# Performance work log

Hardware: AMD Instinct MI355X
Metric: run time of the kernel (lower is better)

Reference implementation:

```python
import jax, jax.numpy as jnp
import numpy as np

B, T, D = 2, 2048, 1024
H = 16
DH = D // H            # 64, per-head dim
C = 128                # d_kv_compress
ROPE_BASE = 10000.0


def _rope_cos_sin(t_len, d_head, dtype):
    # freqs: (T, d_head/2); emb = cat(freqs, freqs) -> (T, d_head)
    inv_freq = 1.0 / (ROPE_BASE ** (jnp.arange(0, d_head, 2, dtype=jnp.float32) / d_head))
    freqs = jnp.arange(t_len, dtype=jnp.float32)[:, None] * inv_freq[None, :]
    emb = jnp.concatenate([freqs, freqs], axis=-1)
    return jnp.cos(emb).astype(dtype), jnp.sin(emb).astype(dtype)


def _rotate_half(x):
    x1, x2 = jnp.split(x, 2, axis=-1)
    return jnp.concatenate([-x2, x1], axis=-1)


def _apply_rope(x, cos, sin):
    # x: (B,H,T,DH); cos/sin: (T,DH)
    return x * cos[None, None] + _rotate_half(x) * sin[None, None]


def setup_inputs() -> dict:
    key = jax.random.key(0)
    ks = jax.random.split(key, 12)
    s = 0.02
    return {
        "x": jax.random.normal(ks[0], (B, T, D), dtype=jnp.float32),
        "w_dk": jax.random.normal(ks[1], (D, C), dtype=jnp.float32) * s,
        "b_dk": jnp.zeros((C,), dtype=jnp.float32),
        "w_dv": jax.random.normal(ks[2], (D, C), dtype=jnp.float32) * s,
        "b_dv": jnp.zeros((C,), dtype=jnp.float32),
        "w_uk": jax.random.normal(ks[3], (C, D), dtype=jnp.float32) * s,
        "b_uk": jnp.zeros((D,), dtype=jnp.float32),
        "w_uv": jax.random.normal(ks[4], (C, D), dtype=jnp.float32) * s,
        "b_uv": jnp.zeros((D,), dtype=jnp.float32),
        "w_o": jax.random.normal(ks[5], (D, D), dtype=jnp.float32) * s,
        "b_o": jnp.zeros((D,), dtype=jnp.float32),
    }


def reference(x, w_dk, b_dk, w_dv, b_dv, w_uk, b_uk, w_uv, b_uv, w_o, b_o):
    Bx, Tx, Dx = x.shape
    # low-rank KV compression then up-projection
    c_k = x @ w_dk + b_dk                      # (B,T,C)
    c_v = x @ w_dv + b_dv                      # (B,T,C)
    k = c_k @ w_uk + b_uk                      # (B,T,D)
    v = c_v @ w_uv + b_uv                      # (B,T,D)

    def split_heads(t):  # (B,T,D) -> (B,H,T,DH)
        return t.reshape(Bx, Tx, H, DH).transpose(0, 2, 1, 3)

    q = split_heads(x)
    k = split_heads(k)
    v = split_heads(v)

    cos, sin = _rope_cos_sin(Tx, DH, x.dtype)
    q = _apply_rope(q, cos, sin)
    k = _apply_rope(k, cos, sin)

    scale = 1.0 / np.sqrt(DH)
    attn = jnp.einsum('bhid,bhjd->bhij', q, k) * scale
    attn = jax.nn.softmax(attn, axis=-1)
    out = jnp.einsum('bhij,bhjd->bhid', attn, v)   # (B,H,T,DH)
    out = out.transpose(0, 2, 1, 3).reshape(Bx, Tx, Dx)
    return out @ w_o + b_o
```

## Files before the change

### kernel.cpp

```cpp
#include <hip/hip_runtime.h>
#include <math.h>

constexpr int kB  = 2;
constexpr int kT  = 2048;
constexpr int kD  = 1024;
constexpr int kH  = 16;
constexpr int kDH = 64;
constexpr int kC  = 128;
constexpr int kM  = kB * kT;
constexpr int kBH = kB * kH;

#define LOG10000_OVER_32 0.28782313662425575f

typedef unsigned short ushort_t;
using short8 = __attribute__((ext_vector_type(8))) short;
using f32x4  = __attribute__((ext_vector_type(4))) float;

__device__ inline ushort_t f2bf(float f) {
    unsigned int u = __float_as_uint(f);
    unsigned int r = (u + 0x7fffu + ((u >> 16) & 1u)) >> 16;
    return (ushort_t)r;
}

__device__ inline short8 cvt8(const float* p) {
    float4 f0 = *reinterpret_cast<const float4*>(p);
    float4 f1 = *reinterpret_cast<const float4*>(p + 4);
    short8 v;
    v[0] = (short)f2bf(f0.x); v[1] = (short)f2bf(f0.y);
    v[2] = (short)f2bf(f0.z); v[3] = (short)f2bf(f0.w);
    v[4] = (short)f2bf(f1.x); v[5] = (short)f2bf(f1.y);
    v[6] = (short)f2bf(f1.z); v[7] = (short)f2bf(f1.w);
    return v;
}

__global__ __launch_bounds__(256)
void wtrans(const float* __restrict__ w_dk, const float* __restrict__ w_dv,
            const float* __restrict__ w_uk, const float* __restrict__ w_uv,
            const float* __restrict__ w_o,
            ushort_t* __restrict__ dkT, ushort_t* __restrict__ dvT,
            ushort_t* __restrict__ ukT, ushort_t* __restrict__ uvT,
            ushort_t* __restrict__ oT) {
    const float* src; ushort_t* dst; int R, C;
    switch (blockIdx.z) {
        case 0: src = w_dk; dst = dkT; R = kD; C = kC; break;
        case 1: src = w_dv; dst = dvT; R = kD; C = kC; break;
        case 2: src = w_uk; dst = ukT; R = kC; C = kD; break;
        case 3: src = w_uv; dst = uvT; R = kC; C = kD; break;
        default: src = w_o; dst = oT;  R = kD; C = kD; break;
    }
    int c0 = blockIdx.x * 32, r0 = blockIdx.y * 32;
    if (c0 >= C || r0 >= R) return;

    __shared__ float Tl[32][33];
    int tx = threadIdx.x & 31, ty = threadIdx.x >> 5;
#pragma unroll
    for (int i = 0; i < 4; ++i)
        Tl[ty + 8 * i][tx] = src[(size_t)(r0 + ty + 8 * i) * C + c0 + tx];
    __syncthreads();
#pragma unroll
    for (int i = 0; i < 4; ++i)
        dst[(size_t)(c0 + ty + 8 * i) * R + r0 + tx] = f2bf(Tl[tx][ty + 8 * i]);
}

template<bool AF32, int MODE0, int MODE1>
__global__ __launch_bounds__(256)
void gemm_mfma(const void* __restrict__ A0_, const void* __restrict__ A1_,
               const ushort_t* __restrict__ Wt0, const float* __restrict__ bias0, void* __restrict__ C0,
               const ushort_t* __restrict__ Wt1, const float* __restrict__ bias1, void* __restrict__ C1,
               int M, int N, int K) {
    constexpr int LDT = 40;
    __shared__ __align__(16) ushort_t As[128 * LDT];
    __shared__ __align__(16) ushort_t Bs[128 * LDT];

    const void*     A    = blockIdx.z ? A1_ : A0_;
    const ushort_t* Wt   = blockIdx.z ? Wt1 : Wt0;
    const float*    bias = blockIdx.z ? bias1 : bias0;
    void*           Cc   = blockIdx.z ? C1 : C0;
    const int       mode = blockIdx.z ? MODE1 : MODE0;

    const int tid  = threadIdx.x;
    const int wave = tid >> 6, lane = tid & 63;
    const int g = lane >> 4, cl = lane & 15;
    const int m0 = blockIdx.y * 128, n0 = blockIdx.x * 128;
    const int wm = (wave >> 1) * 64, wn = (wave & 1) * 64;

    const int ar = tid >> 1;
    const int ac = (tid & 1) * 16;

    f32x4 acc[4][4] = {};

    for (int k0 = 0; k0 < K; k0 += 32) {
        if constexpr (AF32) {
            const float* Af = (const float*)A + (size_t)(m0 + ar) * K + k0 + ac;
            *reinterpret_cast<short8*>(&As[ar * LDT + ac])     = cvt8(Af);
            *reinterpret_cast<short8*>(&As[ar * LDT + ac + 8]) = cvt8(Af + 8);
        } else {
            const ushort_t* Ab = (const ushort_t*)A + (size_t)(m0 + ar) * K + k0 + ac;
            *reinterpret_cast<short8*>(&As[ar * LDT + ac])     = *reinterpret_cast<const short8*>(Ab);
            *reinterpret_cast<short8*>(&As[ar * LDT + ac + 8]) = *reinterpret_cast<const short8*>(Ab + 8);
        }
        {
            const ushort_t* Wb = Wt + (size_t)(n0 + ar) * K + k0 + ac;
            *reinterpret_cast<short8*>(&Bs[ar * LDT + ac])     = *reinterpret_cast<const short8*>(Wb);
            *reinterpret_cast<short8*>(&Bs[ar * LDT + ac + 8]) = *reinterpret_cast<const short8*>(Wb + 8);
        }
        __syncthreads();

        short8 a[4], b[4];
#pragma unroll
        for (int mi = 0; mi < 4; ++mi)
            a[mi] = *reinterpret_cast<const short8*>(&As[(wm + mi * 16 + cl) * LDT + g * 8]);
#pragma unroll
        for (int ni = 0; ni < 4; ++ni)
            b[ni] = *reinterpret_cast<const short8*>(&Bs[(wn + ni * 16 + cl) * LDT + g * 8]);
#pragma unroll
        for (int mi = 0; mi < 4; ++mi)
#pragma unroll
            for (int ni = 0; ni < 4; ++ni)
                acc[mi][ni] = __builtin_amdgcn_mfma_f32_16x16x32_bf16(a[mi], b[ni], acc[mi][ni], 0, 0, 0);
        __syncthreads();
    }

#pragma unroll
    for (int mi = 0; mi < 4; ++mi) {
#pragma unroll
        for (int ni = 0; ni < 4; ++ni) {
            const int mb = m0 + wm + mi * 16 + 4 * g;
            const int nn = n0 + wn + ni * 16 + cl;
            const float bv = bias[nn];
            if (mode == 0) {
#pragma unroll
                for (int r = 0; r < 4; ++r)
                    ((float*)Cc)[(size_t)(mb + r) * N + nn] = acc[mi][ni][r] + bv;
            } else if (mode == 3) {
#pragma unroll
                for (int r = 0; r < 4; ++r)
                    ((ushort_t*)Cc)[(size_t)(mb + r) * N + nn] = f2bf(acc[mi][ni][r] + bv);
            } else if (mode == 1) {
                const int h = nn >> 6, d = nn & (kDH - 1);
#pragma unroll
                for (int r = 0; r < 4; ++r) {
                    int m = mb + r;
                    int bb = m >> 11, t = m & (kT - 1);
                    ((float*)Cc)[(((size_t)bb * kH + h) * kT + t) * kDH + d] = acc[mi][ni][r] + bv;
                }
            } else {
                const int h = nn >> 6, d = nn & (kDH - 1);
                const int bb = mb >> 11, t0 = mb & (kT - 1);
                uint2 u;
                u.x = (unsigned int)f2bf(acc[mi][ni][0] + bv) | ((unsigned int)f2bf(acc[mi][ni][1] + bv) << 16);
                u.y = (unsigned int)f2bf(acc[mi][ni][2] + bv) | ((unsigned int)f2bf(acc[mi][ni][3] + bv) << 16);
                ushort_t* vt = (ushort_t*)Cc;
                *reinterpret_cast<uint2*>(&vt[(((size_t)bb * kH + h) * kDH + d) * kT + t0]) = u;
            }
        }
    }
}

__global__ __launch_bounds__(256)
void rope_split_q(const float* __restrict__ x, ushort_t* __restrict__ q_bf) {
    int idx = blockIdx.x * 256 + threadIdx.x;
    int i = idx & 31;
    int h = (idx >> 5) & (kH - 1);
    int t = (idx >> 9) & (kT - 1);
    int b = idx >> 20;

    const float* xp = x + ((size_t)(b * kT + t)) * kD + h * kDH;
    float x1 = xp[i];
    float x2 = xp[i + 32];

    float inv_freq = expf(-(float)i * LOG10000_OVER_32);
    float ang = (float)t * inv_freq;
    float s, c;
    sincosf(ang, &s, &c);

    ushort_t* qp = q_bf + (((size_t)(b * kH + h)) * kT + t) * kDH;
    qp[i]      = f2bf((x1 * c - x2 * s) * 0.125f);
    qp[i + 32] = f2bf((x2 * c + x1 * s) * 0.125f);
}

__global__ __launch_bounds__(256)
void rope_k_bf(const float* __restrict__ k_r, ushort_t* __restrict__ k_bf) {
    int idx = blockIdx.x * 256 + threadIdx.x;
    int i  = idx & 31;
    int t  = (idx >> 5) & (kT - 1);
    int bh = idx >> 16;

    const float* kp = k_r + ((size_t)bh * kT + t) * kDH;
    float k1 = kp[i];
    float k2 = kp[i + 32];

    float inv_freq = expf(-(float)i * LOG10000_OVER_32);
    float ang = (float)t * inv_freq;
    float s, c;
    sincosf(ang, &s, &c);

    ushort_t* op = k_bf + ((size_t)bh * kT + t) * kDH;
    op[i]      = f2bf(k1 * c - k2 * s);
    op[i + 32] = f2bf(k2 * c + k1 * s);
}

__global__ __launch_bounds__(256)
void attn_mfma(const ushort_t* __restrict__ q_bf, const ushort_t* __restrict__ k_bf,
               const ushort_t* __restrict__ vt_bf, ushort_t* __restrict__ att_bf) {
    constexpr int LDK = 72;
    constexpr int LDV = 40;
    const int blk  = blockIdx.x;
    const int bh   = (blk & 7) * 4 + ((blk >> 3) & 3);
    const int qt   = blk >> 5;
    const int tid  = threadIdx.x;
    const int wave = tid >> 6;
    const int lane = tid & 63;
    const int g = lane >> 4, c = lane & 15;
    const int qbase = qt * 64 + wave * 16;

    __shared__ __align__(16) ushort_t Ks[32 * LDK];
    __shared__ __align__(16) ushort_t Vs[64 * LDV];
    __shared__ __align__(16) ushort_t P_lds[4][16][32];
    ushort_t (*P)[32] = P_lds[wave];

    const ushort_t* qp = q_bf + ((size_t)bh * kT + qbase) * kDH;
    short8 qa0 = *reinterpret_cast<const short8*>(qp + (size_t)c * kDH + g * 8);
    short8 qa1 = *reinterpret_cast<const short8*>(qp + (size_t)c * kDH + g * 8 + 32);

    const ushort_t* kb = k_bf + (size_t)bh * kT * kDH;
    const ushort_t* vb = vt_bf + (size_t)bh * kDH * kT;

    const int kr_ = tid >> 3, kc_ = (tid & 7) * 8;
    const int vr_ = tid >> 2, vc_ = (tid & 3) * 8;

    f32x4 acc[4] = {};
    float lsum[4] = {0.f, 0.f, 0.f, 0.f};

    for (int kt = 0; kt < kT; kt += 32) {
        *reinterpret_cast<short8*>(&Ks[kr_ * LDK + kc_]) =
            *reinterpret_cast<const short8*>(&kb[(size_t)(kt + kr_) * kDH + kc_]);
        *reinterpret_cast<short8*>(&Vs[vr_ * LDV + vc_]) =
            *reinterpret_cast<const short8*>(&vb[(size_t)vr_ * kT + kt + vc_]);
        __syncthreads();

        short8 k00 = *reinterpret_cast<const short8*>(&Ks[c * LDK + g * 8]);
        short8 k01 = *reinterpret_cast<const short8*>(&Ks[c * LDK + 32 + g * 8]);
        short8 k10 = *reinterpret_cast<const short8*>(&Ks[(16 + c) * LDK + g * 8]);
        short8 k11 = *reinterpret_cast<const short8*>(&Ks[(16 + c) * LDK + 32 + g * 8]);

        f32x4 z = {0.f, 0.f, 0.f, 0.f};
        f32x4 s0 = __builtin_amdgcn_mfma_f32_16x16x32_bf16(qa0, k00, z, 0, 0, 0);
        s0 = __builtin_amdgcn_mfma_f32_16x16x32_bf16(qa1, k01, s0, 0, 0, 0);
        f32x4 s1 = __builtin_amdgcn_mfma_f32_16x16x32_bf16(qa0, k10, z, 0, 0, 0);
        s1 = __builtin_amdgcn_mfma_f32_16x16x32_bf16(qa1, k11, s1, 0, 0, 0);

        float p0[4], p1[4];
#pragma unroll
        for (int r = 0; r < 4; ++r) {
            p0[r] = __expf(s0[r]);
            p1[r] = __expf(s1[r]);
            lsum[r] += p0[r] + p1[r];
        }

#pragma unroll
        for (int r = 0; r < 4; ++r) {
            P[4 * g + r][c]      = f2bf(p0[r]);
            P[4 * g + r][16 + c] = f2bf(p1[r]);
        }
        short8 pa = *reinterpret_cast<const short8*>(&P[c][g * 8]);

#pragma unroll
        for (int n = 0; n < 4; ++n) {
            short8 vf = *reinterpret_cast<const short8*>(&Vs[(16 * n + c) * LDV + g * 8]);
            acc[n] = __builtin_amdgcn_mfma_f32_16x16x32_bf16(pa, vf, acc[n], 0, 0, 0);
        }
        __syncthreads();
    }

#pragma unroll
    for (int off = 1; off < 16; off <<= 1)
#pragma unroll
        for (int r = 0; r < 4; ++r) lsum[r] += __shfl_xor(lsum[r], off, 64);

    const int b = bh >> 4, h = bh & (kH - 1);
#pragma unroll
    for (int r = 0; r < 4; ++r) {
        float inv_l = 1.0f / lsum[r];
        size_t row = (size_t)(b * kT + qbase + 4 * g + r) * kD + h * kDH;
#pragma unroll
        for (int n = 0; n < 4; ++n)
            att_bf[row + 16 * n + c] = f2bf(acc[n][r] * inv_l);
    }
}

extern "C" void kernel_launch(void* const* d_in, const int* in_sizes, int n_in,
                              void* d_out, int out_size, void* d_ws, size_t ws_size,
                              hipStream_t stream) {
    const float* x    = (const float*)d_in[0];
    const float* w_dk = (const float*)d_in[1];
    const float* b_dk = (const float*)d_in[2];
    const float* w_dv = (const float*)d_in[3];
    const float* b_dv = (const float*)d_in[4];
    const float* w_uk = (const float*)d_in[5];
    const float* b_uk = (const float*)d_in[6];
    const float* w_uv = (const float*)d_in[7];
    const float* b_uv = (const float*)d_in[8];
    const float* w_o  = (const float*)d_in[9];
    const float* b_o  = (const float*)d_in[10];
    float* out = (float*)d_out;

    char* w = (char*)d_ws;
    float*    k_r    = (float*)w;     w += (size_t)kM * kD * 4;
    ushort_t* q_bf   = (ushort_t*)w;  w += (size_t)kM * kD * 2;
    ushort_t* k_bf   = (ushort_t*)w;  w += (size_t)kM * kD * 2;
    ushort_t* vt_bf  = (ushort_t*)w;  w += (size_t)kM * kD * 2;
    ushort_t* att_bf = (ushort_t*)w;  w += (size_t)kM * kD * 2;
    ushort_t* ckbf   = (ushort_t*)w;  w += (size_t)kM * kC * 2;
    ushort_t* cvbf   = (ushort_t*)w;  w += (size_t)kM * kC * 2;
    ushort_t* dkT    = (ushort_t*)w;  w += (size_t)kC * kD * 2;
    ushort_t* dvT    = (ushort_t*)w;  w += (size_t)kC * kD * 2;
    ushort_t* ukT    = (ushort_t*)w;  w += (size_t)kD * kC * 2;
    ushort_t* uvT    = (ushort_t*)w;  w += (size_t)kD * kC * 2;
    ushort_t* oT     = (ushort_t*)w;  w += (size_t)kD * kD * 2;

    dim3 blk(256);

    wtrans<<<dim3(32, 32, 5), blk, 0, stream>>>(w_dk, w_dv, w_uk, w_uv, w_o,
                                                dkT, dvT, ukT, uvT, oT);

    gemm_mfma<true, 3, 3><<<dim3(kC / 128, kM / 128, 2), blk, 0, stream>>>(
        x, x, dkT, b_dk, ckbf, dvT, b_dv, cvbf, kM, kC, kD);

    gemm_mfma<false, 1, 2><<<dim3(kD / 128, kM / 128, 2), blk, 0, stream>>>(
        ckbf, cvbf, ukT, b_uk, k_r, uvT, b_uv, vt_bf, kM, kD, kC);

    rope_split_q<<<(kB * kT * kH * 32) / 256, blk, 0, stream>>>(x, q_bf);
    rope_k_bf<<<(kB * kH * kT * 32) / 256, blk, 0, stream>>>(k_r, k_bf);

    attn_mfma<<<dim3(kT / 64 * kBH), blk, 0, stream>>>(q_bf, k_bf, vt_bf, att_bf);

    gemm_mfma<false, 0, 0><<<dim3(kD / 128, kM / 128, 1), blk, 0, stream>>>(
        att_bf, att_bf, oT, b_o, out, oT, b_o, out, kM, kD, kD);
}
```

Before: 255.0 us.

## Fuse K RoPE into up-projection epilogue, use sincos table, widen attention tiles

Precomputes a cos/sin table once in the weight-transpose kernel. The K up-projection GEMM now applies RoPE and writes bf16 directly, which removes the fp32 k_r buffer and the separate rope_k kernel. The q scale is folded with log2(e) so softmax can use exp2f. The attention kernel handles 32 query rows per wave (128 per block) so each K/V tile loaded into shared memory is reused twice, and the custom bf16 rounding is replaced by the library conversion. Softmax still skips max subtraction, so overflow risk remains, and the larger per-wave tile adds register pressure.

```diff
diff --git a/kernel.cpp b/kernel.cpp
--- a/kernel.cpp
+++ b/kernel.cpp
@@ -1,4 +1,5 @@
 #include <hip/hip_runtime.h>
+#include <hip/hip_bf16.h>
 #include <math.h>
 
 constexpr int kB  = 2;
@@ -11,15 +12,15 @@
 constexpr int kBH = kB * kH;
 
 #define LOG10000_OVER_32 0.28782313662425575f
+#define QSCALE 0.1803368801111773f
 
 typedef unsigned short ushort_t;
 using short8 = __attribute__((ext_vector_type(8))) short;
 using f32x4  = __attribute__((ext_vector_type(4))) float;
 
 __device__ inline ushort_t f2bf(float f) {
-    unsigned int u = __float_as_uint(f);
-    unsigned int r = (u + 0x7fffu + ((u >> 16) & 1u)) >> 16;
-    return (ushort_t)r;
+    __hip_bfloat16 h = __float2bfloat16(f);
+    return *reinterpret_cast<ushort_t*>(&h);
 }
 
 __device__ inline short8 cvt8(const float* p) {
@@ -39,7 +40,18 @@
             const float* __restrict__ w_o,
             ushort_t* __restrict__ dkT, ushort_t* __restrict__ dvT,
             ushort_t* __restrict__ ukT, ushort_t* __restrict__ uvT,
-            ushort_t* __restrict__ oT) {
+            ushort_t* __restrict__ oT, float2* __restrict__ tab) {
+    if (blockIdx.z == 5) {
+        int flat = blockIdx.y * 32 + blockIdx.x;
+        if (flat >= kT / 8) return;
+        int t = flat * 8 + (threadIdx.x >> 5);
+        int i = threadIdx.x & 31;
+        float inv_freq = expf(-(float)i * LOG10000_OVER_32);
+        float s, c;
+        sincosf((float)t * inv_freq, &s, &c);
+        tab[t * 32 + i] = make_float2(c, s);
+        return;
+    }
     const float* src; ushort_t* dst; int R, C;
     switch (blockIdx.z) {
         case 0: src = w_dk; dst = dkT; R = kD; C = kC; break;
@@ -67,7 +79,7 @@
 void gemm_mfma(const void* __restrict__ A0_, const void* __restrict__ A1_,
                const ushort_t* __restrict__ Wt0, const float* __restrict__ bias0, void* __restrict__ C0,
                const ushort_t* __restrict__ Wt1, const float* __restrict__ bias1, void* __restrict__ C1,
-               int M, int N, int K) {
+               const float2* __restrict__ tab, int M, int N, int K) {
     constexpr int LDT = 40;
     __shared__ __align__(16) ushort_t As[128 * LDT];
     __shared__ __align__(16) ushort_t Bs[128 * LDT];
@@ -123,6 +135,25 @@
 
 #pragma unroll
     for (int mi = 0; mi < 4; ++mi) {
+        if (mode == 4) {
+            const int h = (n0 + wn) >> 6;
+#pragma unroll
+            for (int r = 0; r < 4; ++r) {
+                const int m = m0 + wm + mi * 16 + 4 * g + r;
+                const int bb = m >> 11, t = m & (kT - 1);
+                ushort_t* kp = (ushort_t*)Cc + (((size_t)bb * kH + h) * kT + t) * kDH;
+#pragma unroll
+                for (int pr = 0; pr < 2; ++pr) {
+                    const int i = pr * 16 + cl;
+                    float2 cs = tab[t * 32 + i];
+                    float v1 = acc[mi][pr][r]     + bias[n0 + wn + pr * 16 + cl];
+                    float v2 = acc[mi][pr + 2][r] + bias[n0 + wn + (pr + 2) * 16 + cl];
+                    kp[i]      = f2bf(v1 * cs.x - v2 * cs.y);
+                    kp[i + 32] = f2bf(v2 * cs.x + v1 * cs.y);
+                }
+            }
+            continue;
+        }
 #pragma unroll
         for (int ni = 0; ni < 4; ++ni) {
             const int mb = m0 + wm + mi * 16 + 4 * g;
@@ -136,14 +167,6 @@
 #pragma unroll
                 for (int r = 0; r < 4; ++r)
                     ((ushort_t*)Cc)[(size_t)(mb + r) * N + nn] = f2bf(acc[mi][ni][r] + bv);
-            } else if (mode == 1) {
-                const int h = nn >> 6, d = nn & (kDH - 1);
-#pragma unroll
-                for (int r = 0; r < 4; ++r) {
-                    int m = mb + r;
-                    int bb = m >> 11, t = m & (kT - 1);
-                    ((float*)Cc)[(((size_t)bb * kH + h) * kT + t) * kDH + d] = acc[mi][ni][r] + bv;
-                }
             } else {
                 const int h = nn >> 6, d = nn & (kDH - 1);
                 const int bb = mb >> 11, t0 = mb & (kT - 1);
@@ -158,7 +181,8 @@
 }
 
 __global__ __launch_bounds__(256)
-void rope_split_q(const float* __restrict__ x, ushort_t* __restrict__ q_bf) {
+void rope_split_q(const float* __restrict__ x, const float2* __restrict__ tab,
+                  ushort_t* __restrict__ q_bf) {
     int idx = blockIdx.x * 256 + threadIdx.x;
     int i = idx & 31;
     int h = (idx >> 5) & (kH - 1);
@@ -168,36 +192,11 @@
     const float* xp = x + ((size_t)(b * kT + t)) * kD + h * kDH;
     float x1 = xp[i];
     float x2 = xp[i + 32];
-
-    float inv_freq = expf(-(float)i * LOG10000_OVER_32);
-    float ang = (float)t * inv_freq;
-    float s, c;
-    sincosf(ang, &s, &c);
+    float2 cs = tab[t * 32 + i];
 
     ushort_t* qp = q_bf + (((size_t)(b * kH + h)) * kT + t) * kDH;
-    qp[i]      = f2bf((x1 * c - x2 * s) * 0.125f);
-    qp[i + 32] = f2bf((x2 * c + x1 * s) * 0.125f);
-}
-
-__global__ __launch_bounds__(256)
-void rope_k_bf(const float* __restrict__ k_r, ushort_t* __restrict__ k_bf) {
-    int idx = blockIdx.x * 256 + threadIdx.x;
-    int i  = idx & 31;
-    int t  = (idx >> 5) & (kT - 1);
-    int bh = idx >> 16;
-
-    const float* kp = k_r + ((size_t)bh * kT + t) * kDH;
-    float k1 = kp[i];
-    float k2 = kp[i + 32];
-
-    float inv_freq = expf(-(float)i * LOG10000_OVER_32);
-    float ang = (float)t * inv_freq;
-    float s, c;
-    sincosf(ang, &s, &c);
-
-    ushort_t* op = k_bf + ((size_t)bh * kT + t) * kDH;
-    op[i]      = f2bf(k1 * c - k2 * s);
-    op[i + 32] = f2bf(k2 * c + k1 * s);
+    qp[i]      = f2bf((x1 * cs.x - x2 * cs.y) * QSCALE);
+    qp[i + 32] = f2bf((x2 * cs.x + x1 * cs.y) * QSCALE);
 }
 
 __global__ __launch_bounds__(256)
@@ -205,6 +204,7 @@
                const ushort_t* __restrict__ vt_bf, ushort_t* __restrict__ att_bf) {
     constexpr int LDK = 72;
     constexpr int LDV = 40;
+    constexpr int LDP = 36;
     const int blk  = blockIdx.x;
     const int bh   = (blk & 7) * 4 + ((blk >> 3) & 3);
     const int qt   = blk >> 5;
@@ -212,16 +212,20 @@
     const int wave = tid >> 6;
     const int lane = tid & 63;
     const int g = lane >> 4, c = lane & 15;
-    const int qbase = qt * 64 + wave * 16;
+    const int qbase = qt * 128 + wave * 32;
 
     __shared__ __align__(16) ushort_t Ks[32 * LDK];
     __shared__ __align__(16) ushort_t Vs[64 * LDV];
-    __shared__ __align__(16) ushort_t P_lds[4][16][32];
-    ushort_t (*P)[32] = P_lds[wave];
+    __shared__ __align__(16) ushort_t P_lds[4][32 * LDP];
+    ushort_t* P = P_lds[wave];
 
     const ushort_t* qp = q_bf + ((size_t)bh * kT + qbase) * kDH;
-    short8 qa0 = *reinterpret_cast<const short8*>(qp + (size_t)c * kDH + g * 8);
-    short8 qa1 = *reinterpret_cast<const short8*>(qp + (size_t)c * kDH + g * 8 + 32);
+    short8 qa[2][2];
+#pragma unroll
+    for (int qi = 0; qi < 2; ++qi)
+#pragma unroll
+        for (int f = 0; f < 2; ++f)
+            qa[qi][f] = *reinterpret_cast<const short8*>(qp + (size_t)(qi * 16 + c) * kDH + f * 32 + g * 8);
 
     const ushort_t* kb = k_bf + (size_t)bh * kT * kDH;
     const ushort_t* vb = vt_bf + (size_t)bh * kDH * kT;
@@ -229,8 +233,8 @@
     const int kr_ = tid >> 3, kc_ = (tid & 7) * 8;
     const int vr_ = tid >> 2, vc_ = (tid & 3) * 8;
 
-    f32x4 acc[4] = {};
-    float lsum[4] = {0.f, 0.f, 0.f, 0.f};
+    f32x4 acc[2][4] = {};
+    float lsum[2][4] = {};
 
     for (int kt = 0; kt < kT; kt += 32) {
         *reinterpret_cast<short8*>(&Ks[kr_ * LDK + kc_]) =
@@ -239,54 +243,70 @@
             *reinterpret_cast<const short8*>(&vb[(size_t)vr_ * kT + kt + vc_]);
         __syncthreads();
 
-        short8 k00 = *reinterpret_cast<const short8*>(&Ks[c * LDK + g * 8]);
-        short8 k01 = *reinterpret_cast<const short8*>(&Ks[c * LDK + 32 + g * 8]);
-        short8 k10 = *reinterpret_cast<const short8*>(&Ks[(16 + c) * LDK + g * 8]);
-        short8 k11 = *reinterpret_cast<const short8*>(&Ks[(16 + c) * LDK + 32 + g * 8]);
+        short8 kf[2][2];
+#pragma unroll
+        for (int kj = 0; kj < 2; ++kj)
+#pragma unroll
+            for (int f = 0; f < 2; ++f)
+                kf[kj][f] = *reinterpret_cast<const short8*>(&Ks[(kj * 16 + c) * LDK + f * 32 + g * 8]);
 
         f32x4 z = {0.f, 0.f, 0.f, 0.f};
-        f32x4 s0 = __builtin_amdgcn_mfma_f32_16x16x32_bf16(qa0, k00, z, 0, 0, 0);
-        s0 = __builtin_amdgcn_mfma_f32_16x16x32_bf16(qa1, k01, s0, 0, 0, 0);
-        f32x4 s1 = __builtin_amdgcn_mfma_f32_16x16x32_bf16(qa0, k10, z, 0, 0, 0);
-        s1 = __builtin_amdgcn_mfma_f32_16x16x32_bf16(qa1, k11, s1, 0, 0, 0);
-
-        float p0[4], p1[4];
+        f32x4 s[2][2];
+#pragma unroll
+        for (int qi = 0; qi < 2; ++qi)
+#pragma unroll
+            for (int kj = 0; kj < 2; ++kj) {
+                s[qi][kj] = __builtin_amdgcn_mfma_f32_16x16x32_bf16(qa[qi][0], kf[kj][0], z, 0, 0, 0);
+                s[qi][kj] = __builtin_amdgcn_mfma_f32_16x16x32_bf16(qa[qi][1], kf[kj][1], s[qi][kj], 0, 0, 0);
+            }
+
+#pragma unroll
+        for (int qi = 0; qi < 2; ++qi)
+#pragma unroll
+            for (int kj = 0; kj < 2; ++kj)
+#pragma unroll
+                for (int r = 0; r < 4; ++r) {
+                    float p = exp2f(s[qi][kj][r]);
+                    lsum[qi][r] += p;
+                    P[(qi * 16 + 4 * g + r) * LDP + kj * 16 + c] = f2bf(p);
+                }
+
+        short8 pa[2];
+#pragma unroll
+        for (int qi = 0; qi < 2; ++qi)
+            pa[qi] = *reinterpret_cast<const short8*>(&P[(qi * 16 + c) * LDP + g * 8]);
+
+        short8 vf[4];
+#pragma unroll
+        for (int n = 0; n < 4; ++n)
+            vf[n] = *reinterpret_cast<const short8*>(&Vs[(16 * n + c) * LDV + g * 8]);
+#pragma unroll
+        for (int qi = 0; qi < 2; ++qi)
+#pragma unroll
+            for (int n = 0; n < 4; ++n)
+                acc[qi][n] = __builtin_amdgcn_mfma_f32_16x16x32_bf16(pa[qi], vf[n], acc[qi][n], 0, 0, 0);
+        __syncthreads();
+    }
+
+#pragma unroll
+    for (int off = 1; off < 16; off <<= 1)
+#pragma unroll
+        for (int qi = 0; qi < 2; ++qi)
+#pragma unroll
+            for (int r = 0; r < 4; ++r)
+                lsum[qi][r] += __shfl_xor(lsum[qi][r], off, 64);
+
+    const int b = bh >> 4, h = bh & (kH - 1);
+#pragma unroll
+    for (int qi = 0; qi < 2; ++qi)
 #pragma unroll
         for (int r = 0; r < 4; ++r) {
-            p0[r] = __expf(s0[r]);
-            p1[r] = __expf(s1[r]);
-            lsum[r] += p0[r] + p1[r];
-        }
-
-#pragma unroll
-        for (int r = 0; r < 4; ++r) {
-            P[4 * g + r][c]      = f2bf(p0[r]);
-            P[4 * g + r][16 + c] = f2bf(p1[r]);
-        }
-        short8 pa = *reinterpret_cast<const short8*>(&P[c][g * 8]);
-
-#pragma unroll
-        for (int n = 0; n < 4; ++n) {
-            short8 vf = *reinterpret_cast<const short8*>(&Vs[(16 * n + c) * LDV + g * 8]);
-            acc[n] = __builtin_amdgcn_mfma_f32_16x16x32_bf16(pa, vf, acc[n], 0, 0, 0);
-        }
-        __syncthreads();
-    }
-
-#pragma unroll
-    for (int off = 1; off < 16; off <<= 1)
-#pragma unroll
-        for (int r = 0; r < 4; ++r) lsum[r] += __shfl_xor(lsum[r], off, 64);
-
-    const int b = bh >> 4, h = bh & (kH - 1);
-#pragma unroll
-    for (int r = 0; r < 4; ++r) {
-        float inv_l = 1.0f / lsum[r];
-        size_t row = (size_t)(b * kT + qbase + 4 * g + r) * kD + h * kDH;
-#pragma unroll
-        for (int n = 0; n < 4; ++n)
-            att_bf[row + 16 * n + c] = f2bf(acc[n][r] * inv_l);
-    }
+            float inv_l = 1.0f / lsum[qi][r];
+            size_t row = (size_t)(b * kT + qbase + qi * 16 + 4 * g + r) * kD + h * kDH;
+#pragma unroll
+            for (int n = 0; n < 4; ++n)
+                att_bf[row + 16 * n + c] = f2bf(acc[qi][n][r] * inv_l);
+        }
 }
 
 extern "C" void kernel_launch(void* const* d_in, const int* in_sizes, int n_in,
@@ -306,7 +326,6 @@
     float* out = (float*)d_out;
 
     char* w = (char*)d_ws;
-    float*    k_r    = (float*)w;     w += (size_t)kM * kD * 4;
     ushort_t* q_bf   = (ushort_t*)w;  w += (size_t)kM * kD * 2;
     ushort_t* k_bf   = (ushort_t*)w;  w += (size_t)kM * kD * 2;
     ushort_t* vt_bf  = (ushort_t*)w;  w += (size_t)kM * kD * 2;
@@ -318,23 +337,23 @@
     ushort_t* ukT    = (ushort_t*)w;  w += (size_t)kD * kC * 2;
     ushort_t* uvT    = (ushort_t*)w;  w += (size_t)kD * kC * 2;
     ushort_t* oT     = (ushort_t*)w;  w += (size_t)kD * kD * 2;
+    float2*   tab    = (float2*)w;    w += (size_t)kT * 32 * 8;
 
     dim3 blk(256);
 
-    wtrans<<<dim3(32, 32, 5), blk, 0, stream>>>(w_dk, w_dv, w_uk, w_uv, w_o,
-                                                dkT, dvT, ukT, uvT, oT);
+    wtrans<<<dim3(32, 32, 6), blk, 0, stream>>>(w_dk, w_dv, w_uk, w_uv, w_o,
+                                                dkT, dvT, ukT, uvT, oT, tab);
 
     gemm_mfma<true, 3, 3><<<dim3(kC / 128, kM / 128, 2), blk, 0, stream>>>(
-        x, x, dkT, b_dk, ckbf, dvT, b_dv, cvbf, kM, kC, kD);
-
-    gemm_mfma<false, 1, 2><<<dim3(kD / 128, kM / 128, 2), blk, 0, stream>>>(
-        ckbf, cvbf, ukT, b_uk, k_r, uvT, b_uv, vt_bf, kM, kD, kC);
-
-    rope_split_q<<<(kB * kT * kH * 32) / 256, blk, 0, stream>>>(x, q_bf);
-    rope_k_bf<<<(kB * kH * kT * 32) / 256, blk, 0, stream>>>(k_r, k_bf);
-
-    attn_mfma<<<dim3(kT / 64 * kBH), blk, 0, stream>>>(q_bf, k_bf, vt_bf, att_bf);
+        x, x, dkT, b_dk, ckbf, dvT, b_dv, cvbf, nullptr, kM, kC, kD);
+
+    gemm_mfma<false, 4, 2><<<dim3(kD / 128, kM / 128, 2), blk, 0, stream>>>(
+        ckbf, cvbf, ukT, b_uk, k_bf, uvT, b_uv, vt_bf, tab, kM, kD, kC);
+
+    rope_split_q<<<(kB * kT * kH * 32) / 256, blk, 0, stream>>>(x, tab, q_bf);
+
+    attn_mfma<<<dim3(kT / 128 * kBH), blk, 0, stream>>>(q_bf, k_bf, vt_bf, att_bf);
 
     gemm_mfma<false, 0, 0><<<dim3(kD / 128, kM / 128, 1), blk, 0, stream>>>(
-        att_bf, att_bf, oT, b_o, out, oT, b_o, out, kM, kD, kD);
-}
+        att_bf, att_bf, oT, b_o, out, oT, b_o, out, nullptr, kM, kD, kD);
+}
```

Result: slower. 266.0 us (+4.3%).
